# Kernel optimization log

Measured on AMD Instinct MI355X. Metric: run time of the kernel, lower is better.

## Reference

```python
import jax, jax.numpy as jnp
import numpy as np

B, SQ, SK, D, H, DFF, L = 8, 1024, 1024, 512, 8, 2048, 2
HD = D // H  # head dim = 64
EPS = 1e-5


def _ln(x, g, b):
    mu = jnp.mean(x, axis=-1, keepdims=True)
    var = jnp.mean((x - mu) ** 2, axis=-1, keepdims=True)
    return (x - mu) * jax.lax.rsqrt(var + EPS) * g + b


def setup_inputs() -> dict:
    key = jax.random.key(0)
    ks = jax.random.split(key, 16)
    std = 0.02
    inp = {
        'q': jax.random.normal(ks[0], (B, SQ, D), jnp.float32),
        'k': jax.random.normal(ks[1], (B, SK, D), jnp.float32),
        'v': jax.random.normal(ks[2], (B, SK, D), jnp.float32),
        # per-layer stacked params (weights stored [in, out])
        'WQ': jax.random.normal(ks[3], (L, D, D), jnp.float32) * std,
        'bQ': jnp.zeros((L, D), jnp.float32),
        'WK': jax.random.normal(ks[4], (L, D, D), jnp.float32) * std,
        'bK': jnp.zeros((L, D), jnp.float32),
        'WV': jax.random.normal(ks[5], (L, D, D), jnp.float32) * std,
        'bV': jnp.zeros((L, D), jnp.float32),
        'WO': jax.random.normal(ks[6], (L, D, D), jnp.float32) * std,
        'bO': jnp.zeros((L, D), jnp.float32),
        'Wf1': jax.random.normal(ks[7], (L, D, DFF), jnp.float32) * std,
        'bf1': jnp.zeros((L, DFF), jnp.float32),
        'Wf2': jax.random.normal(ks[8], (L, DFF, D), jnp.float32) * std,
        'bf2': jnp.zeros((L, D), jnp.float32),
        'ln1_g': jnp.ones((L, D), jnp.float32),
        'ln1_b': jnp.zeros((L, D), jnp.float32),
        'ln2_g': jnp.ones((L, D), jnp.float32),
        'ln2_b': jnp.zeros((L, D), jnp.float32),
        'scale': jnp.full((L,), HD ** -0.5, jnp.float32),       # self.scale init
        'extra_scale': jnp.ones((L,), jnp.float32),             # self.extra_scale init
        'gate_attn': jnp.ones((L,), jnp.float32),
        'gate_ffn': jnp.ones((L,), jnp.float32),
    }
    return inp


def reference(q, k, v, WQ, bQ, WK, bK, WV, bV, WO, bO, Wf1, bf1, Wf2, bf2,
              ln1_g, ln1_b, ln2_g, ln2_b, scale, extra_scale, gate_attn, gate_ffn):
    prev = None  # Realformer residual attention scores
    for i in range(L):
        # QKV projections -> [B, H, S, HD]
        qh = (jnp.einsum('bsd,de->bse', q, WQ[i]) + bQ[i]).reshape(B, SQ, H, HD).transpose(0, 2, 1, 3)
        kh = (jnp.einsum('bsd,de->bse', k, WK[i]) + bK[i]).reshape(B, SK, H, HD).transpose(0, 2, 1, 3)
        vh = (jnp.einsum('bsd,de->bse', v, WV[i]) + bV[i]).reshape(B, SK, H, HD).transpose(0, 2, 1, 3)
        eff_scale = scale[i] * jnp.clip(extra_scale[i], 0.01, 50.0)
        scores = jnp.einsum('bhqd,bhkd->bhqk', qh, kh) * eff_scale  # [B,H,SQ,SK]
        if prev is not None:
            scores = scores + prev
        attn = jax.nn.softmax(scores, axis=-1)
        out = jnp.einsum('bhqk,bhkd->bhqd', attn, vh)
        out = out.transpose(0, 2, 1, 3).reshape(B, SQ, D)
        out = jnp.einsum('bsd,de->bse', out, WO[i]) + bO[i]
        # gated residual + post-norm
        q = q + jax.nn.softplus(gate_attn[i]) * out
        q = _ln(q, ln1_g[i], ln1_b[i])
        # FFN (exact gelu like torch default)
        ff = jax.nn.gelu(jnp.einsum('bsd,df->bsf', q, Wf1[i]) + bf1[i], approximate=False)
        ff = jnp.einsum('bsf,fd->bsd', ff, Wf2[i]) + bf2[i]
        q = q + jax.nn.softplus(gate_ffn[i]) * ff
        q = _ln(q, ln2_g[i], ln2_b[i])
        prev = scores
    return q
```

## Files before the change

### kernel.cpp

```cpp
#include <hip/hip_runtime.h>

#define B_   8
#define SQ_  1024
#define SK_  1024
#define D_   512
#define H_   8
#define DFF_ 2048
#define L_   2
#define HD_  64
#define M_   8192

typedef __bf16 bf16;
using bf16x8 = __attribute__((ext_vector_type(8))) __bf16;
using f32x4  = __attribute__((ext_vector_type(4))) float;

__device__ inline f32x4 mfma16(bf16x8 a, bf16x8 b, f32x4 c) {
  return __builtin_amdgcn_mfma_f32_16x16x32_bf16(a, b, c, 0, 0, 0);
}

__device__ __forceinline__ void gl2lds16(const bf16* g, bf16* l) {
  __builtin_amdgcn_global_load_lds(
      (const __attribute__((address_space(1))) void*)g,
      (__attribute__((address_space(3))) void*)l, 16, 0, 0);
}

__device__ __forceinline__ float gelu_fast(float x) {
  float u = 1.5957691216f * (x + 0.044715f * x * x * x);
  return x / (1.0f + __expf(-u));
}

struct TP4 { const float* in[4]; bf16* out[4]; };
__global__ __launch_bounds__(256) void transpose4_k(TP4 p) {
  __shared__ bf16 tile[32][33];
  int z = blockIdx.z, wsel = z >> 1, l = z & 1;
  const float* inp  = p.in[wsel]  + (size_t)l * D_ * D_;
  bf16*        outp = p.out[wsel] + (size_t)l * D_ * D_;
  int c0 = blockIdx.x * 32, r0 = blockIdx.y * 32;
  int tx = threadIdx.x & 31, ty = threadIdx.x >> 5;
#pragma unroll
  for (int i = 0; i < 32; i += 8)
    tile[ty + i][tx] = (bf16)inp[(size_t)(r0 + ty + i) * D_ + c0 + tx];
  __syncthreads();
#pragma unroll
  for (int i = 0; i < 32; i += 8)
    outp[(size_t)(c0 + ty + i) * D_ + r0 + tx] = tile[tx][ty + i];
}

__global__ __launch_bounds__(256) void transpose_k(
    const float* __restrict__ in, bf16* __restrict__ out, int R, int C) {
  __shared__ bf16 tile[32][33];
  const float* inp  = in  + (size_t)blockIdx.z * R * C;
  bf16*        outp = out + (size_t)blockIdx.z * R * C;
  int c0 = blockIdx.x * 32, r0 = blockIdx.y * 32;
  int tx = threadIdx.x & 31, ty = threadIdx.x >> 5;
#pragma unroll
  for (int i = 0; i < 32; i += 8)
    tile[ty + i][tx] = (bf16)inp[(size_t)(r0 + ty + i) * C + c0 + tx];
  __syncthreads();
#pragma unroll
  for (int i = 0; i < 32; i += 8)
    outp[(size_t)(c0 + ty + i) * R + r0 + tx] = tile[tx][ty + i];
}

__global__ __launch_bounds__(256) void f2b3_k(
    const float* __restrict__ a, const float* __restrict__ b,
    const float* __restrict__ c, bf16* __restrict__ oa,
    bf16* __restrict__ ob, bf16* __restrict__ oc) {
  int which = blockIdx.y;
  const float* in = (which == 0) ? a : (which == 1) ? b : c;
  bf16* out = (which == 0) ? oa : (which == 1) ? ob : oc;
  int i = (blockIdx.x * 256 + threadIdx.x) * 4;
  float4 v = *(const float4*)&in[i];
  out[i] = (bf16)v.x; out[i + 1] = (bf16)v.y;
  out[i + 2] = (bf16)v.z; out[i + 3] = (bf16)v.w;
}

template<int BN>
__global__ __launch_bounds__(256) void gemm_t(
    const bf16* __restrict__ A, const bf16* __restrict__ Bt,
    const float* __restrict__ bias, bf16* __restrict__ Cb,
    float* __restrict__ Cf, int Nsz, int Ksz, int gelu) {
  constexpr int NI = BN / 32;
  __shared__ bf16 As[2][128 * 32];
  __shared__ bf16 Bs[2][BN * 32];
  const int tid = threadIdx.x;
  const int m0 = blockIdx.x * 128, n0 = blockIdx.y * BN;
  const int w = tid >> 6, lane = tid & 63, quad = lane >> 4, l16 = lane & 15;
  const int wm = (w & 1) << 6, wn = (w >> 1) * (BN / 2);
  const int r4 = lane >> 2;
  const int k8 = (lane & 3) * 8;
  f32x4 acc[4][NI] = {};

  auto stage = [&](int k0, int buf) {
    gl2lds16(&A[(size_t)(m0 + w * 16 + r4) * Ksz + k0 + k8],
             &As[buf][(w * 16) * 32]);
    gl2lds16(&A[(size_t)(m0 + (w + 4) * 16 + r4) * Ksz + k0 + k8],
             &As[buf][((w + 4) * 16) * 32]);
    gl2lds16(&Bt[(size_t)(n0 + w * 16 + r4) * Ksz + k0 + k8],
             &Bs[buf][(w * 16) * 32]);
    if constexpr (BN == 128)
      gl2lds16(&Bt[(size_t)(n0 + (w + 4) * 16 + r4) * Ksz + k0 + k8],
               &Bs[buf][((w + 4) * 16) * 32]);
  };

  stage(0, 0);
  __syncthreads();
  int buf = 0;
  for (int k0 = 0; k0 < Ksz; k0 += 32, buf ^= 1) {
    if (k0 + 32 < Ksz) stage(k0 + 32, buf ^ 1);
    bf16x8 af[4], bfr[NI];
#pragma unroll
    for (int i = 0; i < 4; i++)
      af[i] = *(const bf16x8*)&As[buf][(wm + i * 16 + l16) * 32 + quad * 8];
#pragma unroll
    for (int i = 0; i < NI; i++)
      bfr[i] = *(const bf16x8*)&Bs[buf][(wn + i * 16 + l16) * 32 + quad * 8];
#pragma unroll
    for (int mi = 0; mi < 4; mi++)
#pragma unroll
      for (int ni = 0; ni < NI; ni++)
        acc[mi][ni] = mfma16(af[mi], bfr[ni], acc[mi][ni]);
    __syncthreads();
  }
#pragma unroll
  for (int mi = 0; mi < 4; mi++)
#pragma unroll
    for (int ni = 0; ni < NI; ni++) {
      int col = n0 + wn + ni * 16 + l16;
      float bv = bias[col];
#pragma unroll
      for (int r = 0; r < 4; r++) {
        int row = m0 + wm + mi * 16 + quad * 4 + r;
        float x = acc[mi][ni][r] + bv;
        if (gelu) x = gelu_fast(x);
        size_t idx = (size_t)row * Nsz + col;
        if (Cb) Cb[idx] = (bf16)x;
        if (Cf) Cf[idx] = x;
      }
    }
}

__global__ __launch_bounds__(256) void vtrans2_k(const bf16* __restrict__ vhh,
                                                 bf16* __restrict__ vt0,
                                                 bf16* __restrict__ vt1) {
  __shared__ bf16 sm[64][72];
  int kt = blockIdx.x, bh = blockIdx.y, z = blockIdx.z;
  int coloff = z ? D_ : 0;
  bf16* vt = z ? vt1 : vt0;
  int b = bh >> 3, h = bh & 7;
  int tid = threadIdx.x;
  for (int c = tid; c < 512; c += 256) {
    int key = c >> 3, off = (c & 7) * 8;
    *(uint4*)&sm[key][off] = *(const uint4*)
        &vhh[(size_t)(b * SK_ + kt * 64 + key) * (2 * D_) + coloff + h * 64 + off];
  }
  __syncthreads();
  for (int c = tid; c < 512; c += 256) {
    int hd = c >> 3, koff = (c & 7) * 8;
    bf16 tmp[8];
#pragma unroll
    for (int j = 0; j < 8; j++) tmp[j] = sm[koff + j][hd];
    *(uint4*)&vt[(size_t)(bh * 64 + hd) * SK_ + kt * 64 + koff] = *(uint4*)tmp;
  }
}

template<bool HAS0>
__global__ __launch_bounds__(256) void attn_t(
    const bf16* __restrict__ qh, const bf16* __restrict__ qh0,
    const bf16* __restrict__ kh, const bf16* __restrict__ kh0, int kstride,
    const bf16* __restrict__ vt, const float* __restrict__ scale,
    const float* __restrict__ extra, int li, bf16* __restrict__ ctx) {
  __shared__ bf16 Ks[2 * 2 * 2048];
  __shared__ bf16 K0s[HAS0 ? 2 * 2 * 2048 : 64];
  __shared__ bf16 Vs[2 * 2 * 2048];
  __shared__ bf16 Ps[4][16 * 72];
  int qt = blockIdx.x, bh = blockIdx.y;
  int b = bh >> 3, h = bh & 7;
  int tid = threadIdx.x, w = tid >> 6, lane = tid & 63;
  int quad = lane >> 4, l16 = lane & 15;
  const int r4 = lane >> 2, c4 = (lane & 3) * 8;
  float eff1 = scale[li] * fminf(fmaxf(extra[li], 0.01f), 50.0f);
  float eff0 = HAS0 ? scale[li - 1] * fminf(fmaxf(extra[li - 1], 0.01f), 50.0f) : 0.f;
  bf16x8 aq[2][2], aq0[2][2];
#pragma unroll
  for (int mi = 0; mi < 2; mi++) {
    int qrow = b * SQ_ + qt * 128 + w * 32 + mi * 16 + l16;
    const bf16* qp = qh + (size_t)qrow * D_ + h * 64 + quad * 8;
    aq[mi][0] = *(const bf16x8*)qp; aq[mi][1] = *(const bf16x8*)(qp + 32);
#pragma unroll
    for (int k2 = 0; k2 < 2; k2++)
#pragma unroll
      for (int j = 0; j < 8; j++)
        aq[mi][k2][j] = (bf16)((float)aq[mi][k2][j] * eff1);
    if constexpr (HAS0) {
      const bf16* qp0 = qh0 + (size_t)qrow * D_ + h * 64 + quad * 8;
      aq0[mi][0] = *(const bf16x8*)qp0; aq0[mi][1] = *(const bf16x8*)(qp0 + 32);
#pragma unroll
      for (int k2 = 0; k2 < 2; k2++)
#pragma unroll
        for (int j = 0; j < 8; j++)
          aq0[mi][k2][j] = (bf16)((float)aq0[mi][k2][j] * eff0);
    }
  }
  bf16x8 ones;
#pragma unroll
  for (int j = 0; j < 8; j++) ones[j] = (bf16)1.0f;

  f32x4 o[2][4] = {};
  f32x4 ol[2] = {};

  auto stage = [&](int kt, int bufi) {
    size_t kg = (size_t)(b * SK_ + kt * 64 + w * 16 + r4) * kstride + h * 64 + c4;
    gl2lds16(&kh[kg],      &Ks[(bufi * 2 + 0) * 2048 + (w * 16) * 32]);
    gl2lds16(&kh[kg + 32], &Ks[(bufi * 2 + 1) * 2048 + (w * 16) * 32]);
    if constexpr (HAS0) {
      gl2lds16(&kh0[kg],      &K0s[(bufi * 2 + 0) * 2048 + (w * 16) * 32]);
      gl2lds16(&kh0[kg + 32], &K0s[(bufi * 2 + 1) * 2048 + (w * 16) * 32]);
    }
    size_t vg = (size_t)(bh * 64 + w * 16 + r4) * SK_ + kt * 64 + c4;
    gl2lds16(&vt[vg],      &Vs[(bufi * 2 + 0) * 2048 + (w * 16) * 32]);
    gl2lds16(&vt[vg + 32], &Vs[(bufi * 2 + 1) * 2048 + (w * 16) * 32]);
  };

  stage(0, 0);
  __syncthreads();
  int buf = 0;
  for (int kt = 0; kt < SK_ / 64; kt++, buf ^= 1) {
    if (kt + 1 < SK_ / 64) stage(kt + 1, buf ^ 1);
    bf16x8 bv[2][4];
#pragma unroll
    for (int kk = 0; kk < 2; kk++)
#pragma unroll
      for (int ni = 0; ni < 4; ni++)
        bv[kk][ni] = *(const bf16x8*)&Vs[kk * 2048 + buf * 4096 +
                                         (ni * 16 + l16) * 32 + quad * 8];
#pragma unroll
    for (int mi = 0; mi < 2; mi++) {
#pragma unroll
      for (int ni = 0; ni < 4; ni++) {
        int ro = (ni * 16 + l16) * 32 + quad * 8;
        f32x4 t = {};
        t = mfma16(aq[mi][0], *(const bf16x8*)&Ks[0 * 2048 + buf * 4096 + ro], t);
        t = mfma16(aq[mi][1], *(const bf16x8*)&Ks[1 * 2048 + buf * 4096 + ro], t);
        if constexpr (HAS0) {
          t = mfma16(aq0[mi][0], *(const bf16x8*)&K0s[0 * 2048 + buf * 4096 + ro], t);
          t = mfma16(aq0[mi][1], *(const bf16x8*)&K0s[1 * 2048 + buf * 4096 + ro], t);
        }
#pragma unroll
        for (int r = 0; r < 4; r++)
          Ps[w][(quad * 4 + r) * 72 + ni * 16 + l16] = (bf16)__expf(t[r]);
      }
#pragma unroll
      for (int kk = 0; kk < 2; kk++) {
        bf16x8 ap = *(const bf16x8*)&Ps[w][l16 * 72 + kk * 32 + quad * 8];
        ol[mi] = mfma16(ap, ones, ol[mi]);
#pragma unroll
        for (int ni = 0; ni < 4; ni++)
          o[mi][ni] = mfma16(ap, bv[kk][ni], o[mi][ni]);
      }
    }
    __syncthreads();
  }
#pragma unroll
  for (int mi = 0; mi < 2; mi++)
#pragma unroll
    for (int ni = 0; ni < 4; ni++)
#pragma unroll
      for (int r = 0; r < 4; r++) {
        int row = b * SQ_ + qt * 128 + w * 32 + mi * 16 + quad * 4 + r;
        ctx[(size_t)row * D_ + h * 64 + ni * 16 + l16] =
            (bf16)(o[mi][ni][r] / ol[mi][r]);
      }
}

__global__ __launch_bounds__(256) void ln_k(
    const float* __restrict__ cur_in, const float* __restrict__ add,
    const float* __restrict__ gate, const float* __restrict__ g,
    const float* __restrict__ bb, float* __restrict__ outf,
    bf16* __restrict__ outb) {
  int row = blockIdx.x, tid = threadIdx.x;
  float gv = gate[0];
  float sp = gv > 20.f ? gv : log1pf(expf(gv));
  size_t base = (size_t)row * D_;
  int c0 = tid * 2;
  float2 c2 = *(const float2*)&cur_in[base + c0];
  float2 a2 = *(const float2*)&add[base + c0];
  float x0 = c2.x + sp * a2.x, x1 = c2.y + sp * a2.y;
  float s = x0 + x1, s2 = x0 * x0 + x1 * x1;
#pragma unroll
  for (int m = 1; m < 64; m <<= 1) {
    s += __shfl_xor(s, m);
    s2 += __shfl_xor(s2, m);
  }
  __shared__ float sa[4], sb[4];
  int w = tid >> 6;
  if ((tid & 63) == 0) { sa[w] = s; sb[w] = s2; }
  __syncthreads();
  s = sa[0] + sa[1] + sa[2] + sa[3];
  s2 = sb[0] + sb[1] + sb[2] + sb[3];
  float mu = s * (1.f / D_);
  float var = s2 * (1.f / D_) - mu * mu;
  float rs = rsqrtf(var + 1e-5f);
  float y0 = (x0 - mu) * rs * g[c0] + bb[c0];
  float y1 = (x1 - mu) * rs * g[c0 + 1] + bb[c0 + 1];
  if (outf) { float2 y; y.x = y0; y.y = y1; *(float2*)&outf[base + c0] = y; }
  if (outb) { outb[base + c0] = (bf16)y0; outb[base + c0 + 1] = (bf16)y1; }
}

extern "C" void kernel_launch(void* const* d_in, const int* in_sizes, int n_in,
                              void* d_out, int out_size, void* d_ws,
                              size_t ws_size, hipStream_t stream) {
  const float* qin = (const float*)d_in[0];
  const float* kin = (const float*)d_in[1];
  const float* vin = (const float*)d_in[2];
  const float* WQ  = (const float*)d_in[3];
  const float* bQ  = (const float*)d_in[4];
  const float* WK  = (const float*)d_in[5];
  const float* bK  = (const float*)d_in[6];
  const float* WV  = (const float*)d_in[7];
  const float* bV  = (const float*)d_in[8];
  const float* WO  = (const float*)d_in[9];
  const float* bO  = (const float*)d_in[10];
  const float* Wf1 = (const float*)d_in[11];
  const float* bf1 = (const float*)d_in[12];
  const float* Wf2 = (const float*)d_in[13];
  const float* bf2 = (const float*)d_in[14];
  const float* l1g = (const float*)d_in[15];
  const float* l1b = (const float*)d_in[16];
  const float* l2g = (const float*)d_in[17];
  const float* l2b = (const float*)d_in[18];
  const float* sc  = (const float*)d_in[19];
  const float* ex  = (const float*)d_in[20];
  const float* ga  = (const float*)d_in[21];
  const float* gf  = (const float*)d_in[22];

  char* p = (char*)d_ws;
  auto alloc = [&](size_t bytes) {
    void* r = (void*)p;
    p += (bytes + 255) & ~(size_t)255;
    return r;
  };
  bf16* WQt  = (bf16*)alloc((size_t)L_ * D_ * D_ * 2);
  bf16* WKt  = (bf16*)alloc((size_t)L_ * D_ * D_ * 2);
  bf16* WVt  = (bf16*)alloc((size_t)L_ * D_ * D_ * 2);
  bf16* WOt  = (bf16*)alloc((size_t)L_ * D_ * D_ * 2);
  bf16* Wf1t = (bf16*)alloc((size_t)L_ * D_ * DFF_ * 2);
  bf16* Wf2t = (bf16*)alloc((size_t)L_ * D_ * DFF_ * 2);
  float* cur  = (float*)alloc((size_t)M_ * D_ * 4);
  bf16* curb  = (bf16*)alloc((size_t)M_ * D_ * 2);
  bf16* qb    = (bf16*)alloc((size_t)M_ * D_ * 2);
  bf16* kb    = (bf16*)alloc((size_t)M_ * D_ * 2);
  bf16* vb    = (bf16*)alloc((size_t)M_ * D_ * 2);
  bf16* khh   = (bf16*)alloc((size_t)M_ * 2 * D_ * 2);
  bf16* vhh   = (bf16*)alloc((size_t)M_ * 2 * D_ * 2);
  bf16* qh0b  = (bf16*)alloc((size_t)M_ * D_ * 2);
  bf16* qh1b  = (bf16*)alloc((size_t)M_ * D_ * 2);
  bf16* vt0   = (bf16*)alloc((size_t)M_ * D_ * 2);
  bf16* vt1   = (bf16*)alloc((size_t)M_ * D_ * 2);
  bf16* ctx   = (bf16*)alloc((size_t)M_ * D_ * 2);
  float* proj = (float*)alloc((size_t)M_ * D_ * 4);
  bf16* ffmid = (bf16*)alloc((size_t)M_ * DFF_ * 2);
  float* ffout = (float*)alloc((size_t)M_ * D_ * 4);

  TP4 tp; tp.in[0] = WQ; tp.in[1] = WK; tp.in[2] = WV; tp.in[3] = WO;
  tp.out[0] = WQt; tp.out[1] = WKt; tp.out[2] = WVt; tp.out[3] = WOt;
  transpose4_k<<<dim3(16, 16, 8), 256, 0, stream>>>(tp);
  transpose_k<<<dim3(DFF_ / 32, D_ / 32, L_), 256, 0, stream>>>(Wf1, Wf1t, D_, DFF_);
  transpose_k<<<dim3(D_ / 32, DFF_ / 32, L_), 256, 0, stream>>>(Wf2, Wf2t, DFF_, D_);
  f2b3_k<<<dim3((M_ * D_) / 1024, 3), 256, 0, stream>>>(qin, kin, vin, qb, kb, vb);

  gemm_t<128><<<dim3(M_ / 128, 8), 256, 0, stream>>>(
      kb, WKt, bK, khh, nullptr, 2 * D_, D_, 0);
  gemm_t<128><<<dim3(M_ / 128, 8), 256, 0, stream>>>(
      vb, WVt, bV, vhh, nullptr, 2 * D_, D_, 0);
  vtrans2_k<<<dim3(SK_ / 64, B_ * H_, 2), 256, 0, stream>>>(vhh, vt0, vt1);
  gemm_t<64><<<dim3(M_ / 128, 8), 256, 0, stream>>>(
      qb, WQt, bQ, qh0b, nullptr, D_, D_, 0);

  for (int li = 0; li < L_; li++) {
    if (li > 0)
      gemm_t<64><<<dim3(M_ / 128, 8), 256, 0, stream>>>(
          curb, WQt + (size_t)li * D_ * D_, bQ + li * D_, qh1b, nullptr, D_, D_, 0);
    if (li == 0)
      attn_t<false><<<dim3(SQ_ / 128, B_ * H_), 256, 0, stream>>>(
          qh0b, qh0b, khh, khh, 2 * D_, vt0, sc, ex, 0, ctx);
    else
      attn_t<true><<<dim3(SQ_ / 128, B_ * H_), 256, 0, stream>>>(
          qh1b, qh0b, khh + (size_t)li * D_, khh, 2 * D_, vt1, sc, ex, 1, ctx);
    gemm_t<64><<<dim3(M_ / 128, 8), 256, 0, stream>>>(
        ctx, WOt + (size_t)li * D_ * D_, bO + li * D_, nullptr, proj, D_, D_, 0);
    ln_k<<<M_, 256, 0, stream>>>((li == 0) ? qin : cur, proj, ga + li,
                                 l1g + li * D_, l1b + li * D_, cur, curb);
    gemm_t<128><<<dim3(M_ / 128, DFF_ / 128), 256, 0, stream>>>(
        curb, Wf1t + (size_t)li * D_ * DFF_, bf1 + li * DFF_, ffmid, nullptr,
        DFF_, D_, 1);
    gemm_t<64><<<dim3(M_ / 128, 8), 256, 0, stream>>>(
        ffmid, Wf2t + (size_t)li * DFF_ * D_, bf2 + li * D_, nullptr, ffout,
        D_, DFF_, 0);
    ln_k<<<M_, 256, 0, stream>>>(cur, ffout, gf + li, l2g + li * D_,
                                 l2b + li * D_,
                                 (li == L_ - 1) ? (float*)d_out : cur,
                                 (li == L_ - 1) ? nullptr : curb);
  }
}
```

Measured before the change: 546.7 us.

## Add 256x256-tile 4-stage pipelined GEMM for KV projections and FFN1

Adds a new 512-thread GEMM kernel with 256x256 output tiles, a 4-stage global-to-LDS async load ring with swizzled LDS layout, and interleaved load/MFMA phases with priority hints. It replaces the K/V projection GEMMs, merged into one launch via a z-dimension, and the FFN up-projection with GELU. The aim is more data reuse per tile and better overlap of loads with MFMA. In exchange the kernel uses more LDS and registers, and the grid holds fewer blocks, which could hurt occupancy or load balance.

```diff
diff --git a/kernel.cpp b/kernel.cpp
--- a/kernel.cpp
+++ b/kernel.cpp
@@ -136,6 +136,111 @@
         size_t idx = (size_t)row * Nsz + col;
         if (Cb) Cb[idx] = (bf16)x;
         if (Cf) Cf[idx] = x;
+      }
+    }
+}
+
+struct G256 { const bf16* A; const bf16* Bt; const float* bias; bf16* C; };
+
+#define MFB(mh) \
+  _Pragma("unroll") \
+  for (int mi = 0; mi < 4; mi++) { \
+    _Pragma("unroll") \
+    for (int ni = 0; ni < 4; ni++) \
+      acc[(mh) * 4 + mi][ni] = mfma16(a[mi], b[ni], acc[(mh) * 4 + mi][ni]); \
+  }
+
+#define PHASE(s, mh, STAGE, VM) \
+  { \
+    if ((mh) == 0) { \
+      a[0] = ldA(s, 0); a[1] = ldA(s, 1); a[2] = ldA(s, 2); a[3] = ldA(s, 3); \
+      b[0] = ldB(s, 0); b[1] = ldB(s, 1); b[2] = ldB(s, 2); b[3] = ldB(s, 3); \
+    } else { \
+      a[0] = ldA(s, 4); a[1] = ldA(s, 5); a[2] = ldA(s, 6); a[3] = ldA(s, 7); \
+    } \
+    STAGE; \
+    VM; \
+    __builtin_amdgcn_s_barrier(); \
+    asm volatile("s_waitcnt lgkmcnt(0)" ::: "memory"); \
+    __builtin_amdgcn_sched_barrier(0); \
+    __builtin_amdgcn_s_setprio(1); \
+    MFB(mh); \
+    __builtin_amdgcn_s_setprio(0); \
+    __builtin_amdgcn_s_barrier(); \
+  }
+
+__global__ __launch_bounds__(512, 2) void gemm256_k(G256 g0, G256 g1,
+                                                    int Nsz, int Ksz,
+                                                    int gelu) {
+  __shared__ bf16 As[4 * 8192];
+  __shared__ bf16 Bs[4 * 8192];
+  const G256 g = blockIdx.z ? g1 : g0;
+  const int tid = threadIdx.x;
+  const int w = tid >> 6, lane = tid & 63;
+  const int quad = lane >> 4, l16 = lane & 15;
+  const int wm = w >> 2, wn = w & 3;
+  const int m0 = blockIdx.x * 256, n0 = blockIdx.y * 256;
+  const int NCH = Ksz >> 5;
+  const int ITERS = NCH >> 2;
+
+  const int srow = tid >> 2;
+  const int ssw = ((tid & 3) ^ (srow & 3) ^ ((srow >> 2) & 3)) << 3;
+  const int swr = ((quad ^ (l16 & 3) ^ (l16 >> 2)) << 3);
+
+  auto stageA = [&](int kc, int s) {
+    const bf16* gp = g.A + (size_t)(m0 + srow) * Ksz + kc * 32 + ssw;
+    gl2lds16(gp, &As[s * 8192 + w * 512]);
+    gl2lds16(gp + (size_t)128 * Ksz, &As[s * 8192 + 4096 + w * 512]);
+  };
+  auto stageB = [&](int kc, int s) {
+    const bf16* gp = g.Bt + (size_t)(n0 + srow) * Ksz + kc * 32 + ssw;
+    gl2lds16(gp, &Bs[s * 8192 + w * 512]);
+    gl2lds16(gp + (size_t)128 * Ksz, &Bs[s * 8192 + 4096 + w * 512]);
+  };
+  auto ldA = [&](int s, int mi) {
+    return *(const bf16x8*)&As[s * 8192 + (wm * 128 + mi * 16 + l16) * 32 + swr];
+  };
+  auto ldB = [&](int s, int ni) {
+    return *(const bf16x8*)&Bs[s * 8192 + (wn * 64 + ni * 16 + l16) * 32 + swr];
+  };
+
+  f32x4 acc[8][4] = {};
+
+  stageA(0, 0); stageB(0, 0);
+  stageA(1, 1); stageB(1, 1);
+  stageA(2, 2); stageB(2, 2);
+  asm volatile("s_waitcnt vmcnt(4)" ::: "memory");
+  __builtin_amdgcn_s_barrier();
+
+  for (int it = 0; it < ITERS; ++it) {
+    const int c = it * 4;
+    const bool last = (it + 1 == ITERS);
+    bf16x8 a[4], b[4];
+    PHASE(0, 0, stageA(c + 3, 3), )
+    PHASE(0, 1, stageB(c + 3, 3), )
+    PHASE(1, 0, if (!last) stageA(c + 4, 0), )
+    PHASE(1, 1, if (!last) stageB(c + 4, 0),
+          if (!last) { asm volatile("s_waitcnt vmcnt(4)" ::: "memory"); }
+          else { asm volatile("s_waitcnt vmcnt(0)" ::: "memory"); })
+    PHASE(2, 0, if (!last) stageA(c + 5, 1), )
+    PHASE(2, 1, if (!last) stageB(c + 5, 1), )
+    PHASE(3, 0, if (!last) stageA(c + 6, 2), )
+    PHASE(3, 1, if (!last) stageB(c + 6, 2),
+          asm volatile("s_waitcnt vmcnt(4)" ::: "memory"))
+  }
+
+#pragma unroll
+  for (int mi = 0; mi < 8; mi++)
+#pragma unroll
+    for (int ni = 0; ni < 4; ni++) {
+      const int col = n0 + wn * 64 + ni * 16 + l16;
+      const float bv = g.bias[col];
+#pragma unroll
+      for (int r = 0; r < 4; r++) {
+        const int row = m0 + wm * 128 + mi * 16 + quad * 4 + r;
+        float x = acc[mi][ni][r] + bv;
+        if (gelu) x = gelu_fast(x);
+        g.C[(size_t)row * Nsz + col] = (bf16)x;
       }
     }
 }
@@ -369,10 +474,10 @@
   transpose_k<<<dim3(D_ / 32, DFF_ / 32, L_), 256, 0, stream>>>(Wf2, Wf2t, DFF_, D_);
   f2b3_k<<<dim3((M_ * D_) / 1024, 3), 256, 0, stream>>>(qin, kin, vin, qb, kb, vb);
 
-  gemm_t<128><<<dim3(M_ / 128, 8), 256, 0, stream>>>(
-      kb, WKt, bK, khh, nullptr, 2 * D_, D_, 0);
-  gemm_t<128><<<dim3(M_ / 128, 8), 256, 0, stream>>>(
-      vb, WVt, bV, vhh, nullptr, 2 * D_, D_, 0);
+  G256 gk; gk.A = kb; gk.Bt = WKt; gk.bias = bK; gk.C = khh;
+  G256 gvv; gvv.A = vb; gvv.Bt = WVt; gvv.bias = bV; gvv.C = vhh;
+  gemm256_k<<<dim3(M_ / 256, (2 * D_) / 256, 2), 512, 0, stream>>>(
+      gk, gvv, 2 * D_, D_, 0);
   vtrans2_k<<<dim3(SK_ / 64, B_ * H_, 2), 256, 0, stream>>>(vhh, vt0, vt1);
   gemm_t<64><<<dim3(M_ / 128, 8), 256, 0, stream>>>(
       qb, WQt, bQ, qh0b, nullptr, D_, D_, 0);
@@ -391,9 +496,10 @@
         ctx, WOt + (size_t)li * D_ * D_, bO + li * D_, nullptr, proj, D_, D_, 0);
     ln_k<<<M_, 256, 0, stream>>>((li == 0) ? qin : cur, proj, ga + li,
                                  l1g + li * D_, l1b + li * D_, cur, curb);
-    gemm_t<128><<<dim3(M_ / 128, DFF_ / 128), 256, 0, stream>>>(
-        curb, Wf1t + (size_t)li * D_ * DFF_, bf1 + li * DFF_, ffmid, nullptr,
-        DFF_, D_, 1);
+    G256 gf1; gf1.A = curb; gf1.Bt = Wf1t + (size_t)li * D_ * DFF_;
+    gf1.bias = bf1 + li * DFF_; gf1.C = ffmid;
+    gemm256_k<<<dim3(M_ / 256, DFF_ / 256, 1), 512, 0, stream>>>(
+        gf1, gf1, DFF_, D_, 1);
     gemm_t<64><<<dim3(M_ / 128, 8), 256, 0, stream>>>(
         ffmid, Wf2t + (size_t)li * DFF_ * D_, bf2 + li * D_, nullptr, ffout,
         D_, DFF_, 0);
```

After: 527.4 us. 1.04x faster.
